# Optimization experiments

Measured on AMD Instinct MI355X. Metric: run time of the kernel, lower is better.

Reference implementation:

```python
import jax, jax.numpy as jnp
import numpy as np

INPUT_SZ, HIDDEN_SZ, OUTPUT_SZ, NUM_LAYERS, EMBED_SZ = 128, 512, 64, 4, 16
SEQ_LEN, BATCH = 128, 256


def setup_inputs() -> dict:
    key = jax.random.key(0)
    ks = jax.random.split(key, 12)
    H, E, L = HIDDEN_SZ, EMBED_SZ, NUM_LAYERS
    s = 0.05
    inp = {
        "input": jax.random.randint(ks[0], (SEQ_LEN, BATCH), 0, INPUT_SZ),
        "embed": jax.random.normal(ks[1], (INPUT_SZ, E), jnp.float32) * s,
        # layer 0 (input dim = E), dims: [dir=2, 4H, in]
        "Wih0": jax.random.normal(ks[2], (2, 4 * H, E), jnp.float32) * s,
        "Whh0": jax.random.normal(ks[3], (2, 4 * H, H), jnp.float32) * s,
        "bih0": jax.random.normal(ks[4], (2, 4 * H), jnp.float32) * s,
        "bhh0": jax.random.normal(ks[5], (2, 4 * H), jnp.float32) * s,
        # layers 1..L-1 (input dim = 2H)
        "Wih": jax.random.normal(ks[6], (L - 1, 2, 4 * H, 2 * H), jnp.float32) * s,
        "Whh": jax.random.normal(ks[7], (L - 1, 2, 4 * H, H), jnp.float32) * s,
        "bih": jax.random.normal(ks[8], (L - 1, 2, 4 * H), jnp.float32) * s,
        "bhh": jax.random.normal(ks[9], (L - 1, 2, 4 * H), jnp.float32) * s,
        "fc_w": jax.random.normal(ks[10], (OUTPUT_SZ, 4 * L * H), jnp.float32) * s,
        "fc_b": jax.random.normal(ks[11], (OUTPUT_SZ,), jnp.float32) * s,
    }
    return inp


def _lstm_forward(tokens, embed, Wih0, Whh0, bih0, bhh0, Wih, Whh, bih, bhh, fc_w, fc_b):
    L, H = NUM_LAYERS, HIDDEN_SZ
    T, B = tokens.shape
    xs = embed[tokens]  # [T, B, E]

    def step(carry, x_t):
        h, c = carry  # each [L, 2, B, H]
        x = x_t       # [B, in_dim]
        new_h, new_c = [], []
        for l in range(L):
            Wi = Wih0 if l == 0 else Wih[l - 1]
            Wh = Whh0 if l == 0 else Whh[l - 1]
            b = (bih0 + bhh0) if l == 0 else (bih[l - 1] + bhh[l - 1])
            # both directions see the same single-timestep input (PyTorch
            # bidirectional LSTM called with seq_len=1 per step)
            gates = (jnp.einsum('bi,dgi->dbg', x, Wi)
                     + jnp.einsum('dbh,dgh->dbg', h[l], Wh)
                     + b[:, None, :])  # [2, B, 4H]
            i_g, f_g, g_g, o_g = jnp.split(gates, 4, axis=-1)
            c_new = jax.nn.sigmoid(f_g) * c[l] + jax.nn.sigmoid(i_g) * jnp.tanh(g_g)
            h_new = jax.nn.sigmoid(o_g) * jnp.tanh(c_new)  # [2, B, H]
            new_h.append(h_new)
            new_c.append(c_new)
            x = jnp.concatenate([h_new[0], h_new[1]], axis=-1)  # [B, 2H]
        return (jnp.stack(new_h), jnp.stack(new_c)), None

    h0 = jnp.zeros((L, 2, B, H), xs.dtype)
    c0 = jnp.zeros((L, 2, B, H), xs.dtype)
    (h, c), _ = jax.lax.scan(step, (h0, c0), xs)

    # PyTorch layout: [2L, B, H], layer-major / direction-minor
    h = h.reshape(2 * L, B, H)
    c = c.reshape(2 * L, B, H)
    hid = jnp.concatenate([h, c], axis=2)                 # [2L, B, 2H]
    hid = hid.transpose(1, 0, 2).reshape(B, 4 * L * H)    # cat over 2L slices on dim 1
    out = hid @ fc_w.T + fc_b
    # dropout is identity at inference
    return jax.nn.softmax(out, axis=1)


def reference(input, embed, Wih0, Whh0, bih0, bhh0, Wih, Whh, bih, bhh, fc_w, fc_b):
    return _lstm_forward(input, embed, Wih0, Whh0, bih0, bhh0, Wih, Whh, bih, bhh, fc_w, fc_b)
```

## Files before the change

### kernel.cpp

```cpp
#include <hip/hip_runtime.h>
#include <hip/hip_cooperative_groups.h>

namespace cg = cooperative_groups;

using short8 = __attribute__((ext_vector_type(8))) short;
using f32x4  = __attribute__((ext_vector_type(4))) float;
using f32x2  = __attribute__((ext_vector_type(2))) float;

static constexpr size_t N_WF0 = (size_t)2*32*8*3*4*512;
static constexpr size_t N_WF1 = (size_t)6*32*8*6*4*512;
static constexpr size_t N_WF  = N_WF0 + N_WF1;
static constexpr size_t N_BSE = (size_t)8*2048;
static constexpr size_t N_XPE = (size_t)128*2*256*8;
static constexpr size_t N_HBE = (size_t)2*8*64*256*8;
static constexpr size_t N_CBE = (size_t)8*256*512;
static constexpr size_t N_FCT = (size_t)8192*64;

static constexpr size_t OFF_WF = 0;
static constexpr size_t OFF_BS = OFF_WF + N_WF*2;
static constexpr size_t OFF_XP = OFF_BS + N_BSE*4;
static constexpr size_t OFF_HB = OFF_XP + N_XPE*2;
static constexpr size_t OFF_CB = OFF_HB + N_HBE*2;
static constexpr size_t OFF_HF = OFF_CB + N_CBE*4;
static constexpr size_t OFF_FC = OFF_HF + N_CBE*4;
static constexpr size_t WS_NEEDED = OFF_FC + N_FCT*4;

__device__ __forceinline__ short f2bf(float f) {
  unsigned u = __float_as_uint(f);
  u += 0x7fff + ((u >> 16) & 1);
  return (short)(u >> 16);
}

__global__ void k_prep_wf(const float* __restrict__ Wih0, const float* __restrict__ Whh0,
                          const float* __restrict__ Wih,  const float* __restrict__ Whh,
                          short* __restrict__ Wf) {
  size_t idx = (size_t)blockIdx.x * blockDim.x + threadIdx.x;
  if (idx >= N_WF) return;
  int j  = (int)(idx & 7);
  int lane = (int)((idx >> 3) & 63);
  int gt = (int)((idx >> 9) & 3);
  int lr = lane & 15, qq = lane >> 4;
  float v;
  if (idx < N_WF0) {
    size_t rest = idx >> 11;
    int sl = (int)(rest % 3); size_t r2 = rest / 3;
    int wvv = (int)(r2 & 7);  size_t r3 = r2 >> 3;
    int ncc = (int)(r3 & 31); int dd = (int)(r3 >> 5);
    int g = gt*512 + ncc*16 + lr;
    int k = (wvv*3 + sl)*32 + qq*8 + j;
    if (k < 16)       v = Wih0[((size_t)dd*2048 + g)*16 + k];
    else if (k < 64)  v = 0.f;
    else if (k < 576) v = Whh0[((size_t)dd*2048 + g)*512 + (k - 64)];
    else              v = 0.f;
  } else {
    size_t u = idx - N_WF0;
    size_t rest = u >> 11;
    int sl = (int)(rest % 6); size_t r2 = rest / 6;
    int wvv = (int)(r2 & 7);  size_t r3 = r2 >> 3;
    int ncc = (int)(r3 & 31); int ldm = (int)(r3 >> 5);
    int g = gt*512 + ncc*16 + lr;
    int k = (wvv*6 + sl)*32 + qq*8 + j;
    if (k < 1024) v = Wih[((size_t)ldm*2048 + g)*1024 + k];
    else          v = Whh[((size_t)ldm*2048 + g)*512 + (k - 1024)];
  }
  Wf[idx] = f2bf(v);
}

__global__ void k_prep_bias(const float* __restrict__ bih0, const float* __restrict__ bhh0,
                            const float* __restrict__ bih, const float* __restrict__ bhh,
                            float* __restrict__ bsum) {
  int idx = blockIdx.x * blockDim.x + threadIdx.x;
  if (idx >= (int)N_BSE) return;
  int g = idx & 2047;
  int dd = (idx >> 11) & 1;
  int ll = idx >> 12;
  float v;
  if (ll == 0) v = bih0[dd*2048 + g] + bhh0[dd*2048 + g];
  else         v = bih[((ll-1)*2 + dd)*2048 + g] + bhh[((ll-1)*2 + dd)*2048 + g];
  bsum[idx] = v;
}

__global__ void k_prep_xp(const int* __restrict__ tok, const float* __restrict__ embed,
                          short* __restrict__ XP) {
  int idx = blockIdx.x * blockDim.x + threadIdx.x;
  if (idx >= (int)N_XPE) return;
  int i  = idx & 7;
  int b  = (idx >> 3) & 255;
  int kg = (idx >> 11) & 1;
  int t  = idx >> 12;
  int k = kg*8 + i;
  XP[idx] = f2bf(embed[tok[t*256 + b]*16 + k]);
}

__global__ void k_prep_fcT(const float* __restrict__ fc_w, float* __restrict__ fcT) {
  int idx = blockIdx.x * blockDim.x + threadIdx.x;
  if (idx >= (int)N_FCT) return;
  int o = idx & 63;
  int k = idx >> 6;
  fcT[idx] = fc_w[o * 8192 + k];
}

__global__ void __launch_bounds__(512, 2)
k_lstm(const short* __restrict__ Wf, const float* __restrict__ bsum,
       const short* __restrict__ XP, short* __restrict__ hb,
       float* __restrict__ cb, float* __restrict__ hf) {
  cg::grid_group grid = cg::this_grid();
  const int blk = blockIdx.x;
  const int ld = blk & 7, nc = blk >> 3;
  const int l = ld >> 1, d = ld & 1;
  const int tid = threadIdx.x;
  const int wv = tid >> 6, lane = tid & 63;
  const int q = lane >> 4, lr = lane & 15;
  const int SLb = (l == 0) ? 3 : 6;
  const size_t HB_LD = 131072;

  __shared__ float red[2][8][4][16][16];

  const int eu  = tid >> 7;
  const int en  = (tid >> 3) & 15;
  const int emh = tid & 7;
  float bias4[4];
  if (tid < 256) {
    #pragma unroll
    for (int gt = 0; gt < 4; ++gt)
      bias4[gt] = bsum[ld*2048 + gt*512 + nc*16 + en];
  }

  short8 wreg[6][4];
  {
    const short* wb = (l == 0)
      ? (Wf + (size_t)(d*32 + nc) * (8*3*4*512) + (size_t)wv * (3*4*512))
      : (Wf + N_WF0 + (size_t)((ld - 2)*32 + nc) * (8*6*4*512) + (size_t)wv * (6*4*512));
    #pragma unroll
    for (int sl = 0; sl < 6; ++sl) {
      #pragma unroll
      for (int gt = 0; gt < 4; ++gt) {
        if (sl < SLb) wreg[sl][gt] = *(const short8*)(wb + (sl*4 + gt)*512 + lane*8);
        else          wreg[sl][gt] = short8{0,0,0,0,0,0,0,0};
      }
    }
  }

  float* cbl = cb + (size_t)ld * (256*512);

  for (int s = 0; s < 131; ++s) {
    const int t = s - l;
    if (t >= 0 && t < 128) {
      const int pt = t & 1, pm = pt ^ 1;
      const short* apl[6];
      #pragma unroll
      for (int sl = 0; sl < 6; ++sl) {
        int S = wv * SLb + sl;
        const short* p; int lo;
        if (l == 0) {
          if (S < 2) { p = XP + (size_t)t * 4096; lo = (q < 1 ? q : 1) * 2048 + lr * 8; }
          else {
            int klb = (S <= 17) ? (4*S - 8) : 0;
            p = hb + (size_t)(pm*8 + ld) * HB_LD + (size_t)klb * 2048;
            lo = q * 2048 + lr * 8;
          }
        } else {
          const int pl0 = ld - 2 - d;
          if (S < 16)      p = hb + (size_t)(pt*8 + pl0    ) * HB_LD + (size_t)(4*S      ) * 2048;
          else if (S < 32) p = hb + (size_t)(pt*8 + pl0 + 1) * HB_LD + (size_t)(4*S - 64 ) * 2048;
          else             p = hb + (size_t)(pm*8 + ld     ) * HB_LD + (size_t)(4*S - 128) * 2048;
          lo = q * 2048 + lr * 8;
        }
        apl[sl] = p + lo;
      }

      short8 a[6][2];
      #pragma unroll
      for (int sl = 0; sl < 6; ++sl)
        if (sl < SLb) {
          a[sl][0] = *(const short8*)(apl[sl]);
          a[sl][1] = *(const short8*)(apl[sl] + 128);
        }

      for (int ro = 0; ro < 8; ++ro) {
        float c0 = 0.f, c1 = 0.f; int b0 = 0, b1 = 0, ej = 0;
        if (tid < 256) {
          ej = nc*16 + en;
          b0 = (ro*2 + eu)*16 + emh*2;
          b1 = b0 + 1;
          c0 = cbl[(size_t)b0*512 + ej];
          c1 = cbl[(size_t)b1*512 + ej];
        }
        f32x4 acc[2][4];
        #pragma unroll
        for (int u = 0; u < 2; ++u)
          #pragma unroll
          for (int gt = 0; gt < 4; ++gt) acc[u][gt] = f32x4{0.f,0.f,0.f,0.f};
        #pragma unroll
        for (int sl = 0; sl < 6; ++sl)
          if (sl < SLb) {
            #pragma unroll
            for (int gt = 0; gt < 4; ++gt) {
              acc[0][gt] = __builtin_amdgcn_mfma_f32_16x16x32_bf16(a[sl][0], wreg[sl][gt], acc[0][gt], 0,0,0);
              acc[1][gt] = __builtin_amdgcn_mfma_f32_16x16x32_bf16(a[sl][1], wreg[sl][gt], acc[1][gt], 0,0,0);
            }
          }
        if (ro < 7) {
          const int mo = (ro + 1) * 256;
          #pragma unroll
          for (int sl = 0; sl < 6; ++sl)
            if (sl < SLb) {
              a[sl][0] = *(const short8*)(apl[sl] + mo);
              a[sl][1] = *(const short8*)(apl[sl] + mo + 128);
            }
        }
        #pragma unroll
        for (int u = 0; u < 2; ++u)
          #pragma unroll
          for (int gt = 0; gt < 4; ++gt)
            *(f32x4*)&red[u][wv][gt][lr][q*4] = acc[u][gt];
        __syncthreads();
        if (tid < 256) {
          float g2[4][2];
          #pragma unroll
          for (int gt = 0; gt < 4; ++gt) {
            f32x2 sum = f32x2{0.f, 0.f};
            #pragma unroll
            for (int w8 = 0; w8 < 8; ++w8)
              sum += *(const f32x2*)&red[eu][w8][gt][en][emh*2];
            g2[gt][0] = sum[0] + bias4[gt];
            g2[gt][1] = sum[1] + bias4[gt];
          }
          short* hw = hb + (size_t)(pt*8 + ld) * HB_LD;
          #pragma unroll
          for (int e = 0; e < 2; ++e) {
            float gi = g2[0][e], gf = g2[1][e], gg = g2[2][e], go = g2[3][e];
            float si = 1.f/(1.f + __expf(-gi));
            float sf = 1.f/(1.f + __expf(-gf));
            float so = 1.f/(1.f + __expf(-go));
            float tg = 1.f - 2.f/(1.f + __expf(2.f*gg));
            float cold = e ? c1 : c0;
            int   b    = e ? b1 : b0;
            float cn = sf * cold + si * tg;
            float tc = 1.f - 2.f/(1.f + __expf(2.f*cn));
            float hn = so * tc;
            cbl[(size_t)b*512 + ej] = cn;
            hw[((size_t)(ej >> 3) * 256 + b) * 8 + (ej & 7)] = f2bf(hn);
            if (t == 127) hf[((size_t)ld*256 + b)*512 + ej] = hn;
          }
        }
        __syncthreads();
      }
    }
    grid.sync();
  }
}

__global__ void __launch_bounds__(256)
k_fc(const float* __restrict__ hf, const float* __restrict__ cb,
     const float* __restrict__ fcT, const float* __restrict__ fc_b,
     float* __restrict__ out) {
  const int tid = threadIdx.x;
  const int o = tid & 63;
  const int qw = tid >> 6;
  const int bi = blockIdx.x * 4 + qw;
  __shared__ float hidc[4][128];
  float acc = 0.f;
  for (int k0 = 0; k0 < 8192; k0 += 128) {
    #pragma unroll
    for (int c = 0; c < 2; ++c) {
      int idx = tid + c * 256;
      int r = idx >> 7, kk = idx & 127;
      int k = k0 + kk;
      int sS = k >> 10, rem = k & 1023, part = rem >> 9, j = rem & 511;
      const float* src = part ? cb : hf;
      hidc[r][kk] = src[((size_t)sS * 256 + (blockIdx.x * 4 + r)) * 512 + j];
    }
    __syncthreads();
    const float* hrow = hidc[qw];
    #pragma unroll 8
    for (int kk = 0; kk < 128; ++kk)
      acc += hrow[kk] * fcT[(size_t)(k0 + kk) * 64 + o];
    __syncthreads();
  }
  float v = acc + fc_b[o];
  float m = v;
  #pragma unroll
  for (int off = 32; off; off >>= 1) m = fmaxf(m, __shfl_xor(m, off, 64));
  float e = __expf(v - m);
  float ssum = e;
  #pragma unroll
  for (int off = 32; off; off >>= 1) ssum += __shfl_xor(ssum, off, 64);
  out[bi * 64 + o] = e / ssum;
}

extern "C" void kernel_launch(void* const* d_in, const int* in_sizes, int n_in,
                              void* d_out, int out_size, void* d_ws, size_t ws_size,
                              hipStream_t stream) {
  const int*   tok   = (const int*)d_in[0];
  const float* embed = (const float*)d_in[1];
  const float* Wih0  = (const float*)d_in[2];
  const float* Whh0  = (const float*)d_in[3];
  const float* bih0  = (const float*)d_in[4];
  const float* bhh0  = (const float*)d_in[5];
  const float* Wih   = (const float*)d_in[6];
  const float* Whh   = (const float*)d_in[7];
  const float* bih   = (const float*)d_in[8];
  const float* bhh   = (const float*)d_in[9];
  const float* fc_w  = (const float*)d_in[10];
  const float* fc_b  = (const float*)d_in[11];
  float* out = (float*)d_out;

  if (ws_size < WS_NEEDED) return;

  char* ws = (char*)d_ws;
  short* Wfb  = (short*)(ws + OFF_WF);
  float* bsum = (float*)(ws + OFF_BS);
  short* XP   = (short*)(ws + OFF_XP);
  short* hbuf = (short*)(ws + OFF_HB);
  float* cbuf = (float*)(ws + OFF_CB);
  float* hfb  = (float*)(ws + OFF_HF);
  float* fcT  = (float*)(ws + OFF_FC);

  hipMemsetAsync(ws + OFF_HB + N_HBE, 0, N_HBE, stream);
  hipMemsetAsync(ws + OFF_CB, 0, N_CBE * 4, stream);

  k_prep_wf  <<<(int)((N_WF  + 255) / 256), 256, 0, stream>>>(Wih0, Whh0, Wih, Whh, Wfb);
  k_prep_bias<<<(int)((N_BSE + 255) / 256), 256, 0, stream>>>(bih0, bhh0, bih, bhh, bsum);
  k_prep_xp  <<<(int)((N_XPE + 255) / 256), 256, 0, stream>>>(tok, embed, XP);
  k_prep_fcT <<<(int)((N_FCT + 255) / 256), 256, 0, stream>>>(fc_w, fcT);

  void* kargs[] = {(void*)&Wfb, (void*)&bsum, (void*)&XP,
                   (void*)&hbuf, (void*)&cbuf, (void*)&hfb};
  hipLaunchCooperativeKernel((void*)k_lstm, dim3(256), dim3(512), kargs, 0, stream);

  k_fc<<<64, 256, 0, stream>>>(hfb, cbuf, fcT, fc_b, out);
}
```

Before: 6.961 ms.

## Replace grid-wide barrier with per-layer dataflow flags between LSTM blocks

Removes the cooperative grid.sync per wavefront step and has each block wait only on counters for the timesteps it depends on: its own layer at t-1, the previous layer at t, and the next layer at t-2 so the double buffer is not overwritten early. Each block increments a per-(layer,dir,timestep) counter after finishing a step. This lets layers run skewed with point-to-point synchronisation instead of a global barrier, at the cost of spin-polling on global atomics and the need for correct acquire/release ordering.

```diff
diff --git a/kernel.cpp b/kernel.cpp
--- a/kernel.cpp
+++ b/kernel.cpp
@@ -1,7 +1,4 @@
 #include <hip/hip_runtime.h>
-#include <hip/hip_cooperative_groups.h>
-
-namespace cg = cooperative_groups;
 
 using short8 = __attribute__((ext_vector_type(8))) short;
 using f32x4  = __attribute__((ext_vector_type(4))) float;
@@ -15,6 +12,7 @@
 static constexpr size_t N_HBE = (size_t)2*8*64*256*8;
 static constexpr size_t N_CBE = (size_t)8*256*512;
 static constexpr size_t N_FCT = (size_t)8192*64;
+static constexpr size_t N_FL  = (size_t)8*128;
 
 static constexpr size_t OFF_WF = 0;
 static constexpr size_t OFF_BS = OFF_WF + N_WF*2;
@@ -23,12 +21,18 @@
 static constexpr size_t OFF_CB = OFF_HB + N_HBE*2;
 static constexpr size_t OFF_HF = OFF_CB + N_CBE*4;
 static constexpr size_t OFF_FC = OFF_HF + N_CBE*4;
-static constexpr size_t WS_NEEDED = OFF_FC + N_FCT*4;
+static constexpr size_t OFF_FL = OFF_FC + N_FCT*4;
+static constexpr size_t WS_NEEDED = OFF_FL + N_FL*4;
 
 __device__ __forceinline__ short f2bf(float f) {
   unsigned u = __float_as_uint(f);
   u += 0x7fff + ((u >> 16) & 1);
   return (short)(u >> 16);
+}
+
+__device__ __forceinline__ void wait_ge(int* f, int target) {
+  while (__hip_atomic_load(f, __ATOMIC_RELAXED, __HIP_MEMORY_SCOPE_AGENT) < target)
+    __builtin_amdgcn_s_sleep(2);
 }
 
 __global__ void k_prep_wf(const float* __restrict__ Wih0, const float* __restrict__ Whh0,
@@ -103,8 +107,7 @@
 __global__ void __launch_bounds__(512, 2)
 k_lstm(const short* __restrict__ Wf, const float* __restrict__ bsum,
        const short* __restrict__ XP, short* __restrict__ hb,
-       float* __restrict__ cb, float* __restrict__ hf) {
-  cg::grid_group grid = cg::this_grid();
+       float* __restrict__ cb, float* __restrict__ hf, int* __restrict__ Fl) {
   const int blk = blockIdx.x;
   const int ld = blk & 7, nc = blk >> 3;
   const int l = ld >> 1, d = ld & 1;
@@ -143,111 +146,124 @@
 
   float* cbl = cb + (size_t)ld * (256*512);
 
-  for (int s = 0; s < 131; ++s) {
-    const int t = s - l;
-    if (t >= 0 && t < 128) {
-      const int pt = t & 1, pm = pt ^ 1;
-      const short* apl[6];
-      #pragma unroll
-      for (int sl = 0; sl < 6; ++sl) {
-        int S = wv * SLb + sl;
-        const short* p; int lo;
-        if (l == 0) {
-          if (S < 2) { p = XP + (size_t)t * 4096; lo = (q < 1 ? q : 1) * 2048 + lr * 8; }
-          else {
-            int klb = (S <= 17) ? (4*S - 8) : 0;
-            p = hb + (size_t)(pm*8 + ld) * HB_LD + (size_t)klb * 2048;
-            lo = q * 2048 + lr * 8;
-          }
-        } else {
-          const int pl0 = ld - 2 - d;
-          if (S < 16)      p = hb + (size_t)(pt*8 + pl0    ) * HB_LD + (size_t)(4*S      ) * 2048;
-          else if (S < 32) p = hb + (size_t)(pt*8 + pl0 + 1) * HB_LD + (size_t)(4*S - 64 ) * 2048;
-          else             p = hb + (size_t)(pm*8 + ld     ) * HB_LD + (size_t)(4*S - 128) * 2048;
+  for (int t = 0; t < 128; ++t) {
+    if (tid == 0) {
+      if (t > 0) wait_ge(Fl + ld*128 + (t-1), 32);
+      if (l > 0) {
+        wait_ge(Fl + (ld-2-d)*128 + t, 32);
+        wait_ge(Fl + (ld-1-d)*128 + t, 32);
+      }
+      if (l < 3 && t >= 2) {
+        wait_ge(Fl + (2*l+2)*128 + (t-2), 32);
+        wait_ge(Fl + (2*l+3)*128 + (t-2), 32);
+      }
+    }
+    __syncthreads();
+    __builtin_amdgcn_fence(__ATOMIC_ACQUIRE, "agent");
+
+    const int pt = t & 1, pm = pt ^ 1;
+    const short* apl[6];
+    #pragma unroll
+    for (int sl = 0; sl < 6; ++sl) {
+      int S = wv * SLb + sl;
+      const short* p; int lo;
+      if (l == 0) {
+        if (S < 2) { p = XP + (size_t)t * 4096; lo = (q < 1 ? q : 1) * 2048 + lr * 8; }
+        else {
+          int klb = (S <= 17) ? (4*S - 8) : 0;
+          p = hb + (size_t)(pm*8 + ld) * HB_LD + (size_t)klb * 2048;
           lo = q * 2048 + lr * 8;
         }
-        apl[sl] = p + lo;
-      }
-
-      short8 a[6][2];
+      } else {
+        const int pl0 = ld - 2 - d;
+        if (S < 16)      p = hb + (size_t)(pt*8 + pl0    ) * HB_LD + (size_t)(4*S      ) * 2048;
+        else if (S < 32) p = hb + (size_t)(pt*8 + pl0 + 1) * HB_LD + (size_t)(4*S - 64 ) * 2048;
+        else             p = hb + (size_t)(pm*8 + ld     ) * HB_LD + (size_t)(4*S - 128) * 2048;
+        lo = q * 2048 + lr * 8;
+      }
+      apl[sl] = p + lo;
+    }
+
+    short8 a[6][2];
+    #pragma unroll
+    for (int sl = 0; sl < 6; ++sl)
+      if (sl < SLb) {
+        a[sl][0] = *(const short8*)(apl[sl]);
+        a[sl][1] = *(const short8*)(apl[sl] + 128);
+      }
+
+    for (int ro = 0; ro < 8; ++ro) {
+      float c0 = 0.f, c1 = 0.f; int b0 = 0, b1 = 0, ej = 0;
+      if (tid < 256) {
+        ej = nc*16 + en;
+        b0 = (ro*2 + eu)*16 + emh*2;
+        b1 = b0 + 1;
+        c0 = cbl[(size_t)b0*512 + ej];
+        c1 = cbl[(size_t)b1*512 + ej];
+      }
+      f32x4 acc[2][4];
+      #pragma unroll
+      for (int u = 0; u < 2; ++u)
+        #pragma unroll
+        for (int gt = 0; gt < 4; ++gt) acc[u][gt] = f32x4{0.f,0.f,0.f,0.f};
       #pragma unroll
       for (int sl = 0; sl < 6; ++sl)
         if (sl < SLb) {
-          a[sl][0] = *(const short8*)(apl[sl]);
-          a[sl][1] = *(const short8*)(apl[sl] + 128);
+          #pragma unroll
+          for (int gt = 0; gt < 4; ++gt) {
+            acc[0][gt] = __builtin_amdgcn_mfma_f32_16x16x32_bf16(a[sl][0], wreg[sl][gt], acc[0][gt], 0,0,0);
+            acc[1][gt] = __builtin_amdgcn_mfma_f32_16x16x32_bf16(a[sl][1], wreg[sl][gt], acc[1][gt], 0,0,0);
+          }
         }
-
-      for (int ro = 0; ro < 8; ++ro) {
-        float c0 = 0.f, c1 = 0.f; int b0 = 0, b1 = 0, ej = 0;
-        if (tid < 256) {
-          ej = nc*16 + en;
-          b0 = (ro*2 + eu)*16 + emh*2;
-          b1 = b0 + 1;
-          c0 = cbl[(size_t)b0*512 + ej];
-          c1 = cbl[(size_t)b1*512 + ej];
-        }
-        f32x4 acc[2][4];
-        #pragma unroll
-        for (int u = 0; u < 2; ++u)
-          #pragma unroll
-          for (int gt = 0; gt < 4; ++gt) acc[u][gt] = f32x4{0.f,0.f,0.f,0.f};
+      if (ro < 7) {
+        const int mo = (ro + 1) * 256;
         #pragma unroll
         for (int sl = 0; sl < 6; ++sl)
           if (sl < SLb) {
-            #pragma unroll
-            for (int gt = 0; gt < 4; ++gt) {
-              acc[0][gt] = __builtin_amdgcn_mfma_f32_16x16x32_bf16(a[sl][0], wreg[sl][gt], acc[0][gt], 0,0,0);
-              acc[1][gt] = __builtin_amdgcn_mfma_f32_16x16x32_bf16(a[sl][1], wreg[sl][gt], acc[1][gt], 0,0,0);
-            }
+            a[sl][0] = *(const short8*)(apl[sl] + mo);
+            a[sl][1] = *(const short8*)(apl[sl] + mo + 128);
           }
-        if (ro < 7) {
-          const int mo = (ro + 1) * 256;
+      }
+      #pragma unroll
+      for (int u = 0; u < 2; ++u)
+        #pragma unroll
+        for (int gt = 0; gt < 4; ++gt)
+          *(f32x4*)&red[u][wv][gt][lr][q*4] = acc[u][gt];
+      __syncthreads();
+      if (tid < 256) {
+        float g2[4][2];
+        #pragma unroll
+        for (int gt = 0; gt < 4; ++gt) {
+          f32x2 sum = f32x2{0.f, 0.f};
           #pragma unroll
-          for (int sl = 0; sl < 6; ++sl)
-            if (sl < SLb) {
-              a[sl][0] = *(const short8*)(apl[sl] + mo);
-              a[sl][1] = *(const short8*)(apl[sl] + mo + 128);
-            }
+          for (int w8 = 0; w8 < 8; ++w8)
+            sum += *(const f32x2*)&red[eu][w8][gt][en][emh*2];
+          g2[gt][0] = sum[0] + bias4[gt];
+          g2[gt][1] = sum[1] + bias4[gt];
         }
-        #pragma unroll
-        for (int u = 0; u < 2; ++u)
-          #pragma unroll
-          for (int gt = 0; gt < 4; ++gt)
-            *(f32x4*)&red[u][wv][gt][lr][q*4] = acc[u][gt];
-        __syncthreads();
-        if (tid < 256) {
-          float g2[4][2];
-          #pragma unroll
-          for (int gt = 0; gt < 4; ++gt) {
-            f32x2 sum = f32x2{0.f, 0.f};
-            #pragma unroll
-            for (int w8 = 0; w8 < 8; ++w8)
-              sum += *(const f32x2*)&red[eu][w8][gt][en][emh*2];
-            g2[gt][0] = sum[0] + bias4[gt];
-            g2[gt][1] = sum[1] + bias4[gt];
-          }
-          short* hw = hb + (size_t)(pt*8 + ld) * HB_LD;
-          #pragma unroll
-          for (int e = 0; e < 2; ++e) {
-            float gi = g2[0][e], gf = g2[1][e], gg = g2[2][e], go = g2[3][e];
-            float si = 1.f/(1.f + __expf(-gi));
-            float sf = 1.f/(1.f + __expf(-gf));
-            float so = 1.f/(1.f + __expf(-go));
-            float tg = 1.f - 2.f/(1.f + __expf(2.f*gg));
-            float cold = e ? c1 : c0;
-            int   b    = e ? b1 : b0;
-            float cn = sf * cold + si * tg;
-            float tc = 1.f - 2.f/(1.f + __expf(2.f*cn));
-            float hn = so * tc;
-            cbl[(size_t)b*512 + ej] = cn;
-            hw[((size_t)(ej >> 3) * 256 + b) * 8 + (ej & 7)] = f2bf(hn);
-            if (t == 127) hf[((size_t)ld*256 + b)*512 + ej] = hn;
-          }
+        short* hw = hb + (size_t)(pt*8 + ld) * HB_LD;
+        #pragma unroll
+        for (int e = 0; e < 2; ++e) {
+          float gi = g2[0][e], gf = g2[1][e], gg = g2[2][e], go = g2[3][e];
+          float si = 1.f/(1.f + __expf(-gi));
+          float sf = 1.f/(1.f + __expf(-gf));
+          float so = 1.f/(1.f + __expf(-go));
+          float tg = 1.f - 2.f/(1.f + __expf(2.f*gg));
+          float cold = e ? c1 : c0;
+          int   b    = e ? b1 : b0;
+          float cn = sf * cold + si * tg;
+          float tc = 1.f - 2.f/(1.f + __expf(2.f*cn));
+          float hn = so * tc;
+          cbl[(size_t)b*512 + ej] = cn;
+          hw[((size_t)(ej >> 3) * 256 + b) * 8 + (ej & 7)] = f2bf(hn);
+          if (t == 127) hf[((size_t)ld*256 + b)*512 + ej] = hn;
         }
-        __syncthreads();
-      }
-    }
-    grid.sync();
+      }
+      __syncthreads();
+    }
+
+    if (tid == 0)
+      __hip_atomic_fetch_add(Fl + ld*128 + t, 1, __ATOMIC_RELEASE, __HIP_MEMORY_SCOPE_AGENT);
   }
 }
 
@@ -316,9 +332,11 @@
   float* cbuf = (float*)(ws + OFF_CB);
   float* hfb  = (float*)(ws + OFF_HF);
   float* fcT  = (float*)(ws + OFF_FC);
+  int*   flg  = (int*)  (ws + OFF_FL);
 
   hipMemsetAsync(ws + OFF_HB + N_HBE, 0, N_HBE, stream);
   hipMemsetAsync(ws + OFF_CB, 0, N_CBE * 4, stream);
+  hipMemsetAsync(ws + OFF_FL, 0, N_FL * 4, stream);
 
   k_prep_wf  <<<(int)((N_WF  + 255) / 256), 256, 0, stream>>>(Wih0, Whh0, Wih, Whh, Wfb);
   k_prep_bias<<<(int)((N_BSE + 255) / 256), 256, 0, stream>>>(bih0, bhh0, bih, bhh, bsum);
@@ -326,7 +344,7 @@
   k_prep_fcT <<<(int)((N_FCT + 255) / 256), 256, 0, stream>>>(fc_w, fcT);
 
   void* kargs[] = {(void*)&Wfb, (void*)&bsum, (void*)&XP,
-                   (void*)&hbuf, (void*)&cbuf, (void*)&hfb};
+                   (void*)&hbuf, (void*)&cbuf, (void*)&hfb, (void*)&flg};
   hipLaunchCooperativeKernel((void*)k_lstm, dim3(256), dim3(512), kargs, 0, stream);
 
   k_fc<<<64, 256, 0, stream>>>(hfb, cbuf, fcT, fc_b, out);
```

After: 6.139 ms. 11.8% less time.
